# Performance work log

Measured on AMD Instinct MI355X. Metric: run time of the kernel, lower is better.

Reference implementation:

```python
import jax, jax.numpy as jnp
import numpy as np

GRID = 270
POOLED = 90
N_ACTIVE = 30000
LEAK = 0.333  # sparseconvnet BatchNormLeakyReLU default leakiness
CH = [(4, 8), (8, 8), (8, 12), (12, 12), (12, 16), (16, 16)]  # resnet block (nIn, nOut)
NIN_IDX = {0: 0, 2: 1, 4: 2}  # blocks whose shortcut is NetworkInNetwork (nIn != nOut)


def _build_rules(coords, grid, f, lo):
    """Submanifold-conv rulebook: (in_idx, out_idx, offset_idx) pairs over active sites."""
    flat = (coords[:, 0] * grid + coords[:, 1]) * grid + coords[:, 2]
    order = np.argsort(flat)
    flat_s = flat[order]
    n = flat_s.shape[0]
    ins, outs, ks = [], [], []
    kk = 0
    for dx in range(lo, lo + f):
        for dy in range(lo, lo + f):
            for dz in range(lo, lo + f):
                nb = coords + np.array([dx, dy, dz])
                valid = np.all((nb >= 0) & (nb < grid), axis=1)
                nbf = (nb[:, 0] * grid + nb[:, 1]) * grid + nb[:, 2]
                pos = np.clip(np.searchsorted(flat_s, nbf), 0, n - 1)
                hit = valid & (flat_s[pos] == nbf)
                outs.append(np.nonzero(hit)[0])
                ins.append(order[pos[hit]])
                ks.append(np.full(outs[-1].shape[0], kk, dtype=np.int64))
                kk += 1
    return (np.concatenate(ins).astype(np.int32),
            np.concatenate(outs).astype(np.int32),
            np.concatenate(ks).astype(np.int32))


def setup_inputs():
    rng = np.random.default_rng(0)
    flat = np.unique(rng.integers(0, GRID ** 3, size=int(N_ACTIVE * 1.2)))[:N_ACTIVE]
    coords = np.stack([flat // (GRID * GRID), (flat // GRID) % GRID, flat % GRID], 1)
    rb1 = _build_rules(coords, GRID, 2, 0)    # SubmanifoldConvolution f=2
    rb2 = _build_rules(coords, GRID, 15, -7)  # SubmanifoldConvolution f=15
    rb3 = _build_rules(coords, GRID, 5, -2)   # SubmanifoldConvolution f=5
    pc = coords // 3                          # MaxPooling(3, 3)
    pf = (pc[:, 0] * POOLED + pc[:, 1]) * POOLED + pc[:, 2]
    upf, pool_seg = np.unique(pf, return_inverse=True)
    pcoords = np.stack([upf // (POOLED * POOLED), (upf // POOLED) % POOLED, upf % POOLED], 1)
    rb90 = _build_rules(pcoords, POOLED, 3, -1)  # resnet submanifold f=3
    N = coords.shape[0]
    nrm = lambda shape, s: jnp.asarray((rng.normal(0.0, s, size=shape)).astype(np.float32))
    g1s = np.zeros((6, 16), np.float32); b1s = np.zeros((6, 16), np.float32)
    g2s = np.zeros((6, 16), np.float32); b2s = np.zeros((6, 16), np.float32)
    Wa = np.zeros((6, 27, 16, 16), np.float32); Wb = np.zeros((6, 27, 16, 16), np.float32)
    Ws = np.zeros((3, 16, 16), np.float32)
    for i, (ci, co) in enumerate(CH):
        g1s[i, :ci] = 1.0 + 0.05 * rng.normal(size=ci)
        b1s[i, :ci] = 0.05 * rng.normal(size=ci)
        g2s[i, :co] = 1.0 + 0.05 * rng.normal(size=co)
        b2s[i, :co] = 0.05 * rng.normal(size=co)
        Wa[i, :, :ci, :co] = rng.normal(0, 1 / np.sqrt(27 * ci), size=(27, ci, co))
        Wb[i, :, :co, :co] = rng.normal(0, 1 / np.sqrt(27 * co), size=(27, co, co))
        if i in NIN_IDX:
            Ws[NIN_IDX[i], :ci, :co] = rng.normal(0, 1 / np.sqrt(ci), size=(ci, co))
    F = 16 * 84 * 84 * 84
    W_lin1 = jnp.asarray(rng.standard_normal((10, F), dtype=np.float32) * np.float32(1.0 / np.sqrt(F)))
    ii = lambda a: jnp.asarray(a, dtype=jnp.int32)
    return {
        'x_feats': nrm((N, 1), 1.0),
        'W1': nrm((8, 1, 16), 0.35),
        'W2': nrm((3375, 16, 16), 1 / np.sqrt(3375 * 16)),
        'W3': nrm((125, 16, 4), 1 / np.sqrt(125 * 16)),
        'g1s': jnp.asarray(g1s), 'b1s': jnp.asarray(b1s),
        'Wa': jnp.asarray(Wa), 'g2s': jnp.asarray(g2s), 'b2s': jnp.asarray(b2s),
        'Wb': jnp.asarray(Wb), 'Ws': jnp.asarray(Ws),
        'gf': nrm((16,), 0.05) + 1.0, 'bf': nrm((16,), 0.05),
        'Wc1': nrm((16, 16, 3, 3, 3), 1 / np.sqrt(16 * 27)),
        'Wc2': nrm((16, 16, 5, 5, 5), 1 / np.sqrt(16 * 125)),
        'g_bn': nrm((16,), 0.05) + 1.0, 'b_bn': nrm((16,), 0.05),
        'W_lin1': W_lin1, 'b_lin1': nrm((10,), 0.02),
        'W_lin2': nrm((2, 10), 0.3), 'b_lin2': nrm((2,), 0.02),
        'rb1_in': ii(rb1[0]), 'rb1_out': ii(rb1[1]), 'rb1_k': ii(rb1[2]),
        'rb2_in': ii(rb2[0]), 'rb2_out': ii(rb2[1]), 'rb2_k': ii(rb2[2]),
        'rb3_in': ii(rb3[0]), 'rb3_out': ii(rb3[1]), 'rb3_k': ii(rb3[2]),
        'pool_seg': ii(pool_seg),
        'rb90_in': ii(rb90[0]), 'rb90_out': ii(rb90[1]), 'rb90_k': ii(rb90[2]),
        'px': ii(pcoords[:, 0]), 'py': ii(pcoords[:, 1]), 'pz': ii(pcoords[:, 2]),
    }


def _subconv(h, W, in_idx, out_idx, k_idx, n_out):
    # gather active-neighbor features, apply per-offset weight, scatter-add to outputs
    contrib = jnp.einsum('pc,pcd->pd', h[in_idx], W[k_idx])
    return jax.ops.segment_sum(contrib, out_idx, num_segments=n_out)


def reference(x_feats, W1, W2, W3, g1s, b1s, Wa, g2s, b2s, Wb, Ws, gf, bf, Wc1, Wc2,
              g_bn, b_bn, W_lin1, b_lin1, W_lin2, b_lin2,
              rb1_in, rb1_out, rb1_k, rb2_in, rb2_out, rb2_k, rb3_in, rb3_out, rb3_k,
              pool_seg, rb90_in, rb90_out, rb90_k, px, py, pz):
    N = x_feats.shape[0]
    Np = px.shape[0]
    h = _subconv(x_feats, W1, rb1_in, rb1_out, rb1_k, N)   # [N,16] subm conv f=2
    h = _subconv(h, W2, rb2_in, rb2_out, rb2_k, N)         # [N,16] subm conv f=15
    h = _subconv(h, W3, rb3_in, rb3_out, rb3_k, N)         # [N,4]  subm conv f=5
    h = jax.ops.segment_max(h, pool_seg, num_segments=Np)  # sparse MaxPooling 3/3 (dropout=identity, eval)
    h = jnp.pad(h, ((0, 0), (0, 12)))                      # pad channels 4->16; pads stay zero
    for i in range(6):                                     # SparseResNet basic blocks (stride 1)
        u = jax.nn.relu(h * g1s[i] + b1s[i])               # BatchNormReLU (inference, stats folded)
        u = _subconv(u, Wa[i], rb90_in, rb90_out, rb90_k, Np)
        u = jax.nn.relu(u * g2s[i] + b2s[i])
        u = _subconv(u, Wb[i], rb90_in, rb90_out, rb90_k, Np)
        sc = h @ Ws[NIN_IDX[i]] if i in NIN_IDX else h     # NiN or identity shortcut
        h = u + sc
    h = jax.nn.relu(h * gf + bf)                           # trailing BatchNormReLU of SparseResNet
    dense = jnp.zeros((16, POOLED, POOLED, POOLED), h.dtype).at[:, px, py, pz].set(h.T)[None]
    dn = ('NCDHW', 'OIDHW', 'NCDHW')
    d = jax.lax.conv_general_dilated(dense, Wc1, (1, 1, 1), 'VALID', dimension_numbers=dn)  # 90->88
    d = jax.lax.conv_general_dilated(d, Wc2, (1, 1, 1), 'VALID', dimension_numbers=dn)      # 88->84
    d = d * g_bn[None, :, None, None, None] + b_bn[None, :, None, None, None]
    d = jnp.where(d > 0, d, LEAK * d)                      # BatchNormLeakyReLU(16)
    mask = jnp.zeros((1, 1, POOLED, POOLED, POOLED), h.dtype).at[0, 0, px, py, pz].set(1.0)
    mask = jax.lax.reduce_window(mask, 0.0, jax.lax.max, (1, 1, 3, 3, 3), (1,) * 5, 'VALID')
    mask = jax.lax.reduce_window(mask, 0.0, jax.lax.max, (1, 1, 5, 5, 5), (1,) * 5, 'VALID')
    d = d * mask                                           # SparseToDense: zeros off active set
    flat = d.reshape(1, 16 * 84 * 84 * 84)
    return (flat @ W_lin1.T + b_lin1) @ W_lin2.T + b_lin2  # [1, 2]
```

## Files before the change

kernel.cpp:

```cpp
#include <hip/hip_runtime.h>
#include <float.h>

#define TPB 256
#define PG 90
#define PG2 8100
#define PG3 729000
#define DA 88
#define DA2 7744
#define DA3 681472
#define DB 84
#define DB2 7056
#define DB3 592704
#define FTOT 9483264
#define LEAKC 0.333f
#define NBF 1120
#define C1Z 22
#define C2Z 21

static __device__ __forceinline__ void atomicMaxF(float* addr, float val) {
    if (val >= 0.f) atomicMax((int*)addr, __float_as_int(val));
    else            atomicMin((unsigned int*)addr, __float_as_uint(val));
}

__global__ void k_hp_init(float* hp, int n16) {
    int t = blockIdx.x * TPB + threadIdx.x;
    if (t < n16) hp[t] = ((t & 15) < 4) ? -FLT_MAX : 0.f;
}

__global__ void k_sub1(const float* __restrict__ x, const float* __restrict__ W,
                       const int* __restrict__ rin, const int* __restrict__ rout,
                       const int* __restrict__ rk, float* __restrict__ y, int P) {
    int t = blockIdx.x * TPB + threadIdx.x;
    if (t >= P * 16) return;
    int p = t >> 4, d = t & 15;
    atomicAdd(&y[rout[p] * 16 + d], x[rin[p]] * W[rk[p] * 16 + d]);
}

__global__ void k_sub16(const float* __restrict__ h, const float* __restrict__ W,
                        const int* __restrict__ rin, const int* __restrict__ rout,
                        const int* __restrict__ rk, float* __restrict__ y, int P) {
    int t = blockIdx.x * TPB + threadIdx.x;
    if (t >= P * 16) return;
    int p = t >> 4, d = t & 15;
    const float* hr = h + rin[p] * 16;
    const float* w  = W + rk[p] * 256 + d;
    float acc = 0.f;
#pragma unroll
    for (int c = 0; c < 16; c++) acc = fmaf(hr[c], w[c * 16], acc);
    atomicAdd(&y[rout[p] * 16 + d], acc);
}

__global__ void k_sub16bn(const float* __restrict__ h, const float* __restrict__ g,
                          const float* __restrict__ b, const float* __restrict__ W,
                          const int* __restrict__ rin, const int* __restrict__ rout,
                          const int* __restrict__ rk, float* __restrict__ y, int P) {
    int t = blockIdx.x * TPB + threadIdx.x;
    if (t >= P * 16) return;
    int p = t >> 4, d = t & 15;
    const float* hr = h + rin[p] * 16;
    const float* w  = W + rk[p] * 256 + d;
    float acc = 0.f;
#pragma unroll
    for (int c = 0; c < 16; c++) {
        float u = fmaxf(fmaf(hr[c], g[c], b[c]), 0.f);
        acc = fmaf(u, w[c * 16], acc);
    }
    atomicAdd(&y[rout[p] * 16 + d], acc);
}

__global__ void k_sub3(const float* __restrict__ h, const float* __restrict__ W,
                       const int* __restrict__ rin, const int* __restrict__ rout,
                       const int* __restrict__ rk, float* __restrict__ y, int P) {
    int t = blockIdx.x * TPB + threadIdx.x;
    if (t >= P * 4) return;
    int p = t >> 2, d = t & 3;
    const float* hr = h + rin[p] * 16;
    const float* w  = W + rk[p] * 64 + d;
    float acc = 0.f;
#pragma unroll
    for (int c = 0; c < 16; c++) acc = fmaf(hr[c], w[c * 4], acc);
    atomicAdd(&y[rout[p] * 4 + d], acc);
}

__global__ void k_pool(const float* __restrict__ h3, const int* __restrict__ seg,
                       float* __restrict__ hp, int N) {
    int t = blockIdx.x * TPB + threadIdx.x;
    if (t >= N * 4) return;
    int p = t >> 2, d = t & 3;
    atomicMaxF(&hp[seg[p] * 16 + d], h3[t]);
}

__global__ void k_resup(const float* __restrict__ cur, float* __restrict__ wbuf,
                        float* __restrict__ vbuf, const float* __restrict__ Ws,
                        float* __restrict__ nxt, int n16) {
    int t = blockIdx.x * TPB + threadIdx.x;
    if (t >= n16) return;
    int p = t >> 4, d = t & 15;
    float sc;
    if (Ws != nullptr) {
        const float* row = cur + p * 16;
        float acc = 0.f;
#pragma unroll
        for (int c = 0; c < 16; c++) acc = fmaf(row[c], Ws[c * 16 + d], acc);
        sc = acc;
    } else {
        sc = cur[t];
    }
    nxt[t] = wbuf[t] + sc;
    wbuf[t] = 0.f;
    vbuf[t] = 0.f;
}

__global__ void k_scatter(const float* __restrict__ h, const float* __restrict__ gf,
                          const float* __restrict__ bf, const int* __restrict__ px,
                          const int* __restrict__ py, const int* __restrict__ pz,
                          float* __restrict__ dense, unsigned char* __restrict__ occ, int n16) {
    int t = blockIdx.x * TPB + threadIdx.x;
    if (t >= n16) return;
    int p = t >> 4, c = t & 15;
    float v = fmaxf(fmaf(h[t], gf[c], bf[c]), 0.f);
    int pos = (px[p] * PG + py[p]) * PG + pz[p];
    dense[c * PG3 + pos] = v;
    if (c == 0) occ[pos] = 1;
}

__global__ __launch_bounds__(TPB) void k_conv1(const float* __restrict__ in,
                                               const float* __restrict__ W,
                                               float* __restrict__ out) {
    __shared__ float wl[432 * 16];
    for (int t = threadIdx.x; t < 432 * 16; t += TPB) {
        int o = t & 15, tap = t >> 4;
        wl[t] = W[o * 432 + tap];
    }
    __syncthreads();
    int idx = blockIdx.x * TPB + threadIdx.x;
    if (idx >= DA2 * C1Z) return;
    int zg = idx % C1Z;
    int y  = (idx / C1Z) % DA;
    int x  = idx / (C1Z * DA);
    int z0 = zg * 4;
    float acc[4][16];
#pragma unroll
    for (int vz = 0; vz < 4; vz++)
#pragma unroll
        for (int o = 0; o < 16; o++) acc[vz][o] = 0.f;
    for (int i = 0; i < 16; i++) {
        const float* ip = in + (size_t)i * PG3;
#pragma unroll
        for (int kd = 0; kd < 3; kd++) {
#pragma unroll
            for (int kh = 0; kh < 3; kh++) {
                const float* row = ip + (x + kd) * PG2 + (y + kh) * PG + z0;
                float4 fa = *(const float4*)row;
                float4 fb = *(const float4*)(row + 4);
                float v[8] = {fa.x, fa.y, fa.z, fa.w, fb.x, fb.y, fb.z, fb.w};
                const float* wr = &wl[((i * 3 + kd) * 3 + kh) * 3 * 16];
#pragma unroll
                for (int kw = 0; kw < 3; kw++) {
                    const float4* wv = (const float4*)&wr[kw * 16];
                    float4 w0 = wv[0], w1 = wv[1], w2 = wv[2], w3 = wv[3];
#pragma unroll
                    for (int vz = 0; vz < 4; vz++) {
                        float val = v[kw + vz];
                        acc[vz][0]  = fmaf(val, w0.x, acc[vz][0]);
                        acc[vz][1]  = fmaf(val, w0.y, acc[vz][1]);
                        acc[vz][2]  = fmaf(val, w0.z, acc[vz][2]);
                        acc[vz][3]  = fmaf(val, w0.w, acc[vz][3]);
                        acc[vz][4]  = fmaf(val, w1.x, acc[vz][4]);
                        acc[vz][5]  = fmaf(val, w1.y, acc[vz][5]);
                        acc[vz][6]  = fmaf(val, w1.z, acc[vz][6]);
                        acc[vz][7]  = fmaf(val, w1.w, acc[vz][7]);
                        acc[vz][8]  = fmaf(val, w2.x, acc[vz][8]);
                        acc[vz][9]  = fmaf(val, w2.y, acc[vz][9]);
                        acc[vz][10] = fmaf(val, w2.z, acc[vz][10]);
                        acc[vz][11] = fmaf(val, w2.w, acc[vz][11]);
                        acc[vz][12] = fmaf(val, w3.x, acc[vz][12]);
                        acc[vz][13] = fmaf(val, w3.y, acc[vz][13]);
                        acc[vz][14] = fmaf(val, w3.z, acc[vz][14]);
                        acc[vz][15] = fmaf(val, w3.w, acc[vz][15]);
                    }
                }
            }
        }
    }
    int base = x * DA2 + y * DA + z0;
#pragma unroll
    for (int o = 0; o < 16; o++) {
        float4 st = {acc[0][o], acc[1][o], acc[2][o], acc[3][o]};
        *(float4*)(out + (size_t)o * DA3 + base) = st;
    }
}

__global__ __launch_bounds__(TPB) void k_conv2(const float* __restrict__ in,
                                               const float* __restrict__ W,
                                               float* __restrict__ out) {
    __shared__ float wl[4 * 125 * 16];
    int idx = blockIdx.x * TPB + threadIdx.x;
    bool valid = idx < DB2 * C2Z;
    int ii = valid ? idx : 0;
    int zg = ii % C2Z;
    int y  = (ii / C2Z) % DB;
    int x  = ii / (C2Z * DB);
    int z0 = zg * 4;
    float acc[4][16];
#pragma unroll
    for (int vz = 0; vz < 4; vz++)
#pragma unroll
        for (int o = 0; o < 16; o++) acc[vz][o] = 0.f;
    for (int ib = 0; ib < 16; ib += 4) {
        __syncthreads();
        for (int t = threadIdx.x; t < 4 * 125 * 16; t += TPB) {
            int o = t & 15;
            int r = t >> 4;
            int tap = r % 125;
            int ci  = r / 125;
            wl[t] = W[o * 2000 + (ib + ci) * 125 + tap];
        }
        __syncthreads();
        for (int ci = 0; ci < 4; ci++) {
            const float* ip = in + (size_t)(ib + ci) * DA3;
#pragma unroll
            for (int kd = 0; kd < 5; kd++) {
#pragma unroll
                for (int kh = 0; kh < 5; kh++) {
                    const float* row = ip + (x + kd) * DA2 + (y + kh) * DA + z0;
                    float4 fa = *(const float4*)row;
                    float4 fb = *(const float4*)(row + 4);
                    float v[8] = {fa.x, fa.y, fa.z, fa.w, fb.x, fb.y, fb.z, fb.w};
                    const float* wr = &wl[(ci * 125 + kd * 25 + kh * 5) * 16];
#pragma unroll
                    for (int kw = 0; kw < 5; kw++) {
                        const float4* wv = (const float4*)&wr[kw * 16];
                        float4 w0 = wv[0], w1 = wv[1], w2 = wv[2], w3 = wv[3];
#pragma unroll
                        for (int vz = 0; vz < 4; vz++) {
                            float val = v[kw + vz];
                            acc[vz][0]  = fmaf(val, w0.x, acc[vz][0]);
                            acc[vz][1]  = fmaf(val, w0.y, acc[vz][1]);
                            acc[vz][2]  = fmaf(val, w0.z, acc[vz][2]);
                            acc[vz][3]  = fmaf(val, w0.w, acc[vz][3]);
                            acc[vz][4]  = fmaf(val, w1.x, acc[vz][4]);
                            acc[vz][5]  = fmaf(val, w1.y, acc[vz][5]);
                            acc[vz][6]  = fmaf(val, w1.z, acc[vz][6]);
                            acc[vz][7]  = fmaf(val, w1.w, acc[vz][7]);
                            acc[vz][8]  = fmaf(val, w2.x, acc[vz][8]);
                            acc[vz][9]  = fmaf(val, w2.y, acc[vz][9]);
                            acc[vz][10] = fmaf(val, w2.z, acc[vz][10]);
                            acc[vz][11] = fmaf(val, w2.w, acc[vz][11]);
                            acc[vz][12] = fmaf(val, w3.x, acc[vz][12]);
                            acc[vz][13] = fmaf(val, w3.y, acc[vz][13]);
                            acc[vz][14] = fmaf(val, w3.z, acc[vz][14]);
                            acc[vz][15] = fmaf(val, w3.w, acc[vz][15]);
                        }
                    }
                }
            }
        }
    }
    if (valid) {
        int base = x * DB2 + y * DB + z0;
#pragma unroll
        for (int o = 0; o < 16; o++) {
            float4 st = {acc[0][o], acc[1][o], acc[2][o], acc[3][o]};
            *(float4*)(out + (size_t)o * DB3 + base) = st;
        }
    }
}

__global__ void k_mask1(const unsigned char* __restrict__ occ, unsigned char* __restrict__ m1) {
    int t = blockIdx.x * TPB + threadIdx.x;
    if (t >= PG * PG * DB) return;
    int z = t % DB;
    int xy = t / DB;
    const unsigned char* p = occ + xy * PG + z;
    unsigned char m = 0;
#pragma unroll
    for (int k = 0; k < 7; k++) m |= p[k];
    m1[t] = m;
}
__global__ void k_mask2(const unsigned char* __restrict__ m1, unsigned char* __restrict__ m2) {
    int t = blockIdx.x * TPB + threadIdx.x;
    if (t >= PG * DB * DB) return;
    int z = t % DB;
    int y = (t / DB) % DB;
    int x = t / (DB * DB);
    unsigned char m = 0;
#pragma unroll
    for (int k = 0; k < 7; k++) m |= m1[(x * PG + y + k) * DB + z];
    m2[t] = m;
}
__global__ void k_mask3(const unsigned char* __restrict__ m2, unsigned char* __restrict__ mask) {
    int t = blockIdx.x * TPB + threadIdx.x;
    if (t >= DB3) return;
    int z = t % DB;
    int y = (t / DB) % DB;
    int x = t / DB2;
    unsigned char m = 0;
#pragma unroll
    for (int k = 0; k < 7; k++) m |= m2[((x + k) * DB + y) * DB + z];
    mask[t] = m;
}

__global__ __launch_bounds__(TPB) void k_final(const float* __restrict__ c2,
                                               const unsigned char* __restrict__ mask,
                                               const float* __restrict__ gbn,
                                               const float* __restrict__ bbn,
                                               const float* __restrict__ Wl1,
                                               float* __restrict__ buf) {
    int tid0 = blockIdx.x * TPB + threadIdx.x;
    int stride = gridDim.x * TPB;
    float part[10];
#pragma unroll
    for (int j = 0; j < 10; j++) part[j] = 0.f;
    for (int c = 0; c < 16; c++) {
        float g = gbn[c], b = bbn[c];
        const float* cc = c2 + (size_t)c * DB3;
        const float* wb = Wl1 + (size_t)c * DB3;
        for (int sp = tid0; sp < DB3; sp += stride) {
            float v = fmaf(cc[sp], g, b);
            v = v > 0.f ? v : LEAKC * v;
            if (mask[sp]) {
#pragma unroll
                for (int j = 0; j < 10; j++)
                    part[j] = fmaf(v, wb[(size_t)j * FTOT + sp], part[j]);
            }
        }
    }
    int lane = threadIdx.x & 63, wv = threadIdx.x >> 6;
    __shared__ float red[4][10];
#pragma unroll
    for (int j = 0; j < 10; j++) {
        float s = part[j];
#pragma unroll
        for (int off = 32; off; off >>= 1) s += __shfl_down(s, off);
        if (lane == 0) red[wv][j] = s;
    }
    __syncthreads();
    if (threadIdx.x < 10)
        buf[blockIdx.x * 10 + threadIdx.x] =
            red[0][threadIdx.x] + red[1][threadIdx.x] + red[2][threadIdx.x] + red[3][threadIdx.x];
}

__global__ __launch_bounds__(TPB) void k_reduce(const float* __restrict__ buf,
                                                const float* __restrict__ bl1,
                                                float* __restrict__ out10, int nb) {
    int j = blockIdx.x;
    float s = 0.f;
    for (int k = threadIdx.x; k < nb; k += TPB) s += buf[k * 10 + j];
    int lane = threadIdx.x & 63, wv = threadIdx.x >> 6;
#pragma unroll
    for (int off = 32; off; off >>= 1) s += __shfl_down(s, off);
    __shared__ float red[4];
    if (lane == 0) red[wv] = s;
    __syncthreads();
    if (threadIdx.x == 0) out10[j] = red[0] + red[1] + red[2] + red[3] + bl1[j];
}

__global__ void k_head(const float* __restrict__ out10, const float* __restrict__ Wl2,
                       const float* __restrict__ bl2, float* __restrict__ out) {
    if (threadIdx.x == 0) {
        float t0 = bl2[0], t1 = bl2[1];
#pragma unroll
        for (int j = 0; j < 10; j++) {
            float v = out10[j];
            t0 = fmaf(v, Wl2[j], t0);
            t1 = fmaf(v, Wl2[10 + j], t1);
        }
        out[0] = t0;
        out[1] = t1;
    }
}

static inline int nblk(long n) { return (int)((n + TPB - 1) / TPB); }

extern "C" void kernel_launch(void* const* d_in, const int* in_sizes, int n_in,
                              void* d_out, int out_size, void* d_ws, size_t ws_size,
                              hipStream_t stream) {
    const float* x    = (const float*)d_in[0];
    const float* W1   = (const float*)d_in[1];
    const float* W2   = (const float*)d_in[2];
    const float* W3   = (const float*)d_in[3];
    const float* g1s  = (const float*)d_in[4];
    const float* b1s  = (const float*)d_in[5];
    const float* Wa   = (const float*)d_in[6];
    const float* g2s  = (const float*)d_in[7];
    const float* b2s  = (const float*)d_in[8];
    const float* Wb   = (const float*)d_in[9];
    const float* Ws   = (const float*)d_in[10];
    const float* gf   = (const float*)d_in[11];
    const float* bfv  = (const float*)d_in[12];
    const float* Wc1  = (const float*)d_in[13];
    const float* Wc2  = (const float*)d_in[14];
    const float* g_bn = (const float*)d_in[15];
    const float* b_bn = (const float*)d_in[16];
    const float* Wl1  = (const float*)d_in[17];
    const float* bl1  = (const float*)d_in[18];
    const float* Wl2  = (const float*)d_in[19];
    const float* bl2  = (const float*)d_in[20];
    const int* rb1_in = (const int*)d_in[21];
    const int* rb1_out= (const int*)d_in[22];
    const int* rb1_k  = (const int*)d_in[23];
    const int* rb2_in = (const int*)d_in[24];
    const int* rb2_out= (const int*)d_in[25];
    const int* rb2_k  = (const int*)d_in[26];
    const int* rb3_in = (const int*)d_in[27];
    const int* rb3_out= (const int*)d_in[28];
    const int* rb3_k  = (const int*)d_in[29];
    const int* pseg   = (const int*)d_in[30];
    const int* rb9_in = (const int*)d_in[31];
    const int* rb9_out= (const int*)d_in[32];
    const int* rb9_k  = (const int*)d_in[33];
    const int* px     = (const int*)d_in[34];
    const int* py     = (const int*)d_in[35];
    const int* pz     = (const int*)d_in[36];

    const int N   = in_sizes[0];
    const int P1  = in_sizes[21];
    const int P2  = in_sizes[24];
    const int P3  = in_sizes[27];
    const int P90 = in_sizes[31];
    const int Np  = in_sizes[34];

    char* wsp = (char*)d_ws;
    size_t off = 0;
    auto carve = [&](size_t bytes) -> char* {
        char* p = wsp + off;
        off = (off + bytes + 255) & ~(size_t)255;
        return p;
    };
    float* h1    = (float*)carve((size_t)N * 16 * 4);
    float* h2    = (float*)carve((size_t)N * 16 * 4);
    float* h3    = (float*)carve((size_t)N * 4 * 4);
    float* hpA   = (float*)carve((size_t)Np * 16 * 4);
    float* hpB   = (float*)carve((size_t)Np * 16 * 4);
    float* vbuf  = (float*)carve((size_t)Np * 16 * 4);
    float* wbuf  = (float*)carve((size_t)Np * 16 * 4);
    float* dense = (float*)carve((size_t)16 * PG3 * 4);
    float* c1    = (float*)carve((size_t)16 * DA3 * 4);
    unsigned char* occ  = (unsigned char*)carve(PG3);
    unsigned char* m1   = (unsigned char*)carve((size_t)PG * PG * DB);
    unsigned char* m2   = (unsigned char*)carve((size_t)PG * DB * DB);
    unsigned char* mask = (unsigned char*)carve(DB3);
    float* fbuf  = (float*)carve((size_t)NBF * 10 * 4);
    float* out10 = (float*)carve(10 * 4);
    float* c2 = dense;

    hipMemsetAsync(h1, 0, (size_t)N * 16 * 4, stream);
    hipMemsetAsync(h2, 0, (size_t)N * 16 * 4, stream);
    hipMemsetAsync(h3, 0, (size_t)N * 4 * 4, stream);
    hipMemsetAsync(vbuf, 0, (size_t)Np * 16 * 4, stream);
    hipMemsetAsync(wbuf, 0, (size_t)Np * 16 * 4, stream);
    hipMemsetAsync(dense, 0, (size_t)16 * PG3 * 4, stream);
    hipMemsetAsync(occ, 0, PG3, stream);
    k_hp_init<<<nblk((long)Np * 16), TPB, 0, stream>>>(hpA, Np * 16);

    k_sub1<<<nblk((long)P1 * 16), TPB, 0, stream>>>(x, W1, rb1_in, rb1_out, rb1_k, h1, P1);
    k_sub16<<<nblk((long)P2 * 16), TPB, 0, stream>>>(h1, W2, rb2_in, rb2_out, rb2_k, h2, P2);
    k_sub3<<<nblk((long)P3 * 4), TPB, 0, stream>>>(h2, W3, rb3_in, rb3_out, rb3_k, h3, P3);
    k_pool<<<nblk((long)N * 4), TPB, 0, stream>>>(h3, pseg, hpA, N);

    float* cur = hpA;
    float* nxt = hpB;
    for (int i = 0; i < 6; i++) {
        const float* WsP = nullptr;
        if (i == 0) WsP = Ws;
        else if (i == 2) WsP = Ws + 256;
        else if (i == 4) WsP = Ws + 512;
        k_sub16bn<<<nblk((long)P90 * 16), TPB, 0, stream>>>(
            cur, g1s + i * 16, b1s + i * 16, Wa + (size_t)i * 6912,
            rb9_in, rb9_out, rb9_k, vbuf, P90);
        k_sub16bn<<<nblk((long)P90 * 16), TPB, 0, stream>>>(
            vbuf, g2s + i * 16, b2s + i * 16, Wb + (size_t)i * 6912,
            rb9_in, rb9_out, rb9_k, wbuf, P90);
        k_resup<<<nblk((long)Np * 16), TPB, 0, stream>>>(cur, wbuf, vbuf, WsP, nxt, Np * 16);
        float* tmp = cur; cur = nxt; nxt = tmp;
    }

    k_scatter<<<nblk((long)Np * 16), TPB, 0, stream>>>(cur, gf, bfv, px, py, pz, dense, occ, Np * 16);
    k_conv1<<<nblk((long)DA2 * C1Z), TPB, 0, stream>>>(dense, Wc1, c1);
    k_conv2<<<nblk((long)DB2 * C2Z), TPB, 0, stream>>>(c1, Wc2, c2);

    k_mask1<<<nblk((long)PG * PG * DB), TPB, 0, stream>>>(occ, m1);
    k_mask2<<<nblk((long)PG * DB * DB), TPB, 0, stream>>>(m1, m2);
    k_mask3<<<nblk(DB3), TPB, 0, stream>>>(m2, mask);

    k_final<<<NBF, TPB, 0, stream>>>(c2, mask, g_bn, b_bn, Wl1, fbuf);
    k_reduce<<<10, TPB, 0, stream>>>(fbuf, bl1, out10, NBF);
    k_head<<<1, 64, 0, stream>>>(out10, Wl2, bl2, (float*)d_out);
}
```

Baseline: 1.411 ms.

## Split dense convs into two output-channel halves, read pre-permuted weights from global

Both dense 3D convolutions now launch twice as many threads, each computing 8 output channels instead of 16, which halves the accumulator registers per thread and should allow higher occupancy. Weights are permuted once by a new small kernel into tap-major order and read straight from global memory (through cache) instead of being staged in shared memory. This removes the per-block shared-memory fill and barriers. In exchange, every input voxel row is loaded twice (once per half), and the inner loop issues more global weight loads.

```diff
diff --git a/kernel.cpp b/kernel.cpp
--- a/kernel.cpp
+++ b/kernel.cpp
@@ -27,6 +27,13 @@
     if (t < n16) hp[t] = ((t & 15) < 4) ? -FLT_MAX : 0.f;
 }
 
+__global__ void k_permW(const float* __restrict__ W, float* __restrict__ Wp, int ntap) {
+    int t = blockIdx.x * TPB + threadIdx.x;
+    if (t >= ntap * 16) return;
+    int o = t & 15, tap = t >> 4;
+    Wp[t] = W[o * ntap + tap];
+}
+
 __global__ void k_sub1(const float* __restrict__ x, const float* __restrict__ W,
                        const int* __restrict__ rin, const int* __restrict__ rout,
                        const int* __restrict__ rk, float* __restrict__ y, int P) {
@@ -125,59 +132,47 @@
 }
 
 __global__ __launch_bounds__(TPB) void k_conv1(const float* __restrict__ in,
-                                               const float* __restrict__ W,
+                                               const float* __restrict__ Wp,
                                                float* __restrict__ out) {
-    __shared__ float wl[432 * 16];
-    for (int t = threadIdx.x; t < 432 * 16; t += TPB) {
-        int o = t & 15, tap = t >> 4;
-        wl[t] = W[o * 432 + tap];
-    }
-    __syncthreads();
     int idx = blockIdx.x * TPB + threadIdx.x;
-    if (idx >= DA2 * C1Z) return;
-    int zg = idx % C1Z;
-    int y  = (idx / C1Z) % DA;
-    int x  = idx / (C1Z * DA);
+    if (idx >= DA2 * C1Z * 2) return;
+    int oh   = idx / (DA2 * C1Z);
+    int idx2 = idx % (DA2 * C1Z);
+    int zg = idx2 % C1Z;
+    int y  = (idx2 / C1Z) % DA;
+    int x  = idx2 / (C1Z * DA);
     int z0 = zg * 4;
-    float acc[4][16];
+    float acc[4][8];
 #pragma unroll
     for (int vz = 0; vz < 4; vz++)
 #pragma unroll
-        for (int o = 0; o < 16; o++) acc[vz][o] = 0.f;
-    for (int i = 0; i < 16; i++) {
-        const float* ip = in + (size_t)i * PG3;
-#pragma unroll
+        for (int o = 0; o < 8; o++) acc[vz][o] = 0.f;
+    const float* wbase = Wp + oh * 8;
+    for (int ci = 0; ci < 16; ci++) {
+        const float* ip = in + (size_t)ci * PG3 + x * PG2 + y * PG + z0;
+        const float* wc = wbase + ci * 27 * 16;
         for (int kd = 0; kd < 3; kd++) {
-#pragma unroll
             for (int kh = 0; kh < 3; kh++) {
-                const float* row = ip + (x + kd) * PG2 + (y + kh) * PG + z0;
+                const float* row = ip + kd * PG2 + kh * PG;
                 float4 fa = *(const float4*)row;
                 float4 fb = *(const float4*)(row + 4);
                 float v[8] = {fa.x, fa.y, fa.z, fa.w, fb.x, fb.y, fb.z, fb.w};
-                const float* wr = &wl[((i * 3 + kd) * 3 + kh) * 3 * 16];
+                const float* wr = wc + (kd * 9 + kh * 3) * 16;
 #pragma unroll
                 for (int kw = 0; kw < 3; kw++) {
-                    const float4* wv = (const float4*)&wr[kw * 16];
-                    float4 w0 = wv[0], w1 = wv[1], w2 = wv[2], w3 = wv[3];
+                    float4 w0 = *(const float4*)(wr + kw * 16);
+                    float4 w1 = *(const float4*)(wr + kw * 16 + 4);
 #pragma unroll
                     for (int vz = 0; vz < 4; vz++) {
                         float val = v[kw + vz];
-                        acc[vz][0]  = fmaf(val, w0.x, acc[vz][0]);
-                        acc[vz][1]  = fmaf(val, w0.y, acc[vz][1]);
-                        acc[vz][2]  = fmaf(val, w0.z, acc[vz][2]);
-                        acc[vz][3]  = fmaf(val, w0.w, acc[vz][3]);
-                        acc[vz][4]  = fmaf(val, w1.x, acc[vz][4]);
-                        acc[vz][5]  = fmaf(val, w1.y, acc[vz][5]);
-                        acc[vz][6]  = fmaf(val, w1.z, acc[vz][6]);
-                        acc[vz][7]  = fmaf(val, w1.w, acc[vz][7]);
-                        acc[vz][8]  = fmaf(val, w2.x, acc[vz][8]);
-                        acc[vz][9]  = fmaf(val, w2.y, acc[vz][9]);
-                        acc[vz][10] = fmaf(val, w2.z, acc[vz][10]);
-                        acc[vz][11] = fmaf(val, w2.w, acc[vz][11]);
-                        acc[vz][12] = fmaf(val, w3.x, acc[vz][12]);
-                        acc[vz][13] = fmaf(val, w3.y, acc[vz][13]);
-                        acc[vz][14] = fmaf(val, w3.z, acc[vz][14]);
-                        acc[vz][15] = fmaf(val, w3.w, acc[vz][15]);
+                        acc[vz][0] = fmaf(val, w0.x, acc[vz][0]);
+                        acc[vz][1] = fmaf(val, w0.y, acc[vz][1]);
+                        acc[vz][2] = fmaf(val, w0.z, acc[vz][2]);
+                        acc[vz][3] = fmaf(val, w0.w, acc[vz][3]);
+                        acc[vz][4] = fmaf(val, w1.x, acc[vz][4]);
+                        acc[vz][5] = fmaf(val, w1.y, acc[vz][5]);
+                        acc[vz][6] = fmaf(val, w1.z, acc[vz][6]);
+                        acc[vz][7] = fmaf(val, w1.w, acc[vz][7]);
                     }
                 }
             }
@@ -185,85 +180,64 @@
     }
     int base = x * DA2 + y * DA + z0;
 #pragma unroll
-    for (int o = 0; o < 16; o++) {
+    for (int o = 0; o < 8; o++) {
         float4 st = {acc[0][o], acc[1][o], acc[2][o], acc[3][o]};
-        *(float4*)(out + (size_t)o * DA3 + base) = st;
+        *(float4*)(out + (size_t)(oh * 8 + o) * DA3 + base) = st;
     }
 }
 
 __global__ __launch_bounds__(TPB) void k_conv2(const float* __restrict__ in,
-                                               const float* __restrict__ W,
+                                               const float* __restrict__ Wp,
                                                float* __restrict__ out) {
-    __shared__ float wl[4 * 125 * 16];
     int idx = blockIdx.x * TPB + threadIdx.x;
-    bool valid = idx < DB2 * C2Z;
-    int ii = valid ? idx : 0;
-    int zg = ii % C2Z;
-    int y  = (ii / C2Z) % DB;
-    int x  = ii / (C2Z * DB);
+    if (idx >= DB2 * C2Z * 2) return;
+    int oh   = idx / (DB2 * C2Z);
+    int idx2 = idx % (DB2 * C2Z);
+    int zg = idx2 % C2Z;
+    int y  = (idx2 / C2Z) % DB;
+    int x  = idx2 / (C2Z * DB);
     int z0 = zg * 4;
-    float acc[4][16];
+    float acc[4][8];
 #pragma unroll
     for (int vz = 0; vz < 4; vz++)
 #pragma unroll
-        for (int o = 0; o < 16; o++) acc[vz][o] = 0.f;
-    for (int ib = 0; ib < 16; ib += 4) {
-        __syncthreads();
-        for (int t = threadIdx.x; t < 4 * 125 * 16; t += TPB) {
-            int o = t & 15;
-            int r = t >> 4;
-            int tap = r % 125;
-            int ci  = r / 125;
-            wl[t] = W[o * 2000 + (ib + ci) * 125 + tap];
-        }
-        __syncthreads();
-        for (int ci = 0; ci < 4; ci++) {
-            const float* ip = in + (size_t)(ib + ci) * DA3;
-#pragma unroll
-            for (int kd = 0; kd < 5; kd++) {
-#pragma unroll
-                for (int kh = 0; kh < 5; kh++) {
-                    const float* row = ip + (x + kd) * DA2 + (y + kh) * DA + z0;
-                    float4 fa = *(const float4*)row;
-                    float4 fb = *(const float4*)(row + 4);
-                    float v[8] = {fa.x, fa.y, fa.z, fa.w, fb.x, fb.y, fb.z, fb.w};
-                    const float* wr = &wl[(ci * 125 + kd * 25 + kh * 5) * 16];
-#pragma unroll
-                    for (int kw = 0; kw < 5; kw++) {
-                        const float4* wv = (const float4*)&wr[kw * 16];
-                        float4 w0 = wv[0], w1 = wv[1], w2 = wv[2], w3 = wv[3];
-#pragma unroll
-                        for (int vz = 0; vz < 4; vz++) {
-                            float val = v[kw + vz];
-                            acc[vz][0]  = fmaf(val, w0.x, acc[vz][0]);
-                            acc[vz][1]  = fmaf(val, w0.y, acc[vz][1]);
-                            acc[vz][2]  = fmaf(val, w0.z, acc[vz][2]);
-                            acc[vz][3]  = fmaf(val, w0.w, acc[vz][3]);
-                            acc[vz][4]  = fmaf(val, w1.x, acc[vz][4]);
-                            acc[vz][5]  = fmaf(val, w1.y, acc[vz][5]);
-                            acc[vz][6]  = fmaf(val, w1.z, acc[vz][6]);
-                            acc[vz][7]  = fmaf(val, w1.w, acc[vz][7]);
-                            acc[vz][8]  = fmaf(val, w2.x, acc[vz][8]);
-                            acc[vz][9]  = fmaf(val, w2.y, acc[vz][9]);
-                            acc[vz][10] = fmaf(val, w2.z, acc[vz][10]);
-                            acc[vz][11] = fmaf(val, w2.w, acc[vz][11]);
-                            acc[vz][12] = fmaf(val, w3.x, acc[vz][12]);
-                            acc[vz][13] = fmaf(val, w3.y, acc[vz][13]);
-                            acc[vz][14] = fmaf(val, w3.z, acc[vz][14]);
-                            acc[vz][15] = fmaf(val, w3.w, acc[vz][15]);
-                        }
+        for (int o = 0; o < 8; o++) acc[vz][o] = 0.f;
+    const float* wbase = Wp + oh * 8;
+    for (int ci = 0; ci < 16; ci++) {
+        const float* ip = in + (size_t)ci * DA3 + x * DA2 + y * DA + z0;
+        const float* wc = wbase + ci * 125 * 16;
+        for (int kd = 0; kd < 5; kd++) {
+            for (int kh = 0; kh < 5; kh++) {
+                const float* row = ip + kd * DA2 + kh * DA;
+                float4 fa = *(const float4*)row;
+                float4 fb = *(const float4*)(row + 4);
+                float v[8] = {fa.x, fa.y, fa.z, fa.w, fb.x, fb.y, fb.z, fb.w};
+                const float* wr = wc + (kd * 25 + kh * 5) * 16;
+#pragma unroll
+                for (int kw = 0; kw < 5; kw++) {
+                    float4 w0 = *(const float4*)(wr + kw * 16);
+                    float4 w1 = *(const float4*)(wr + kw * 16 + 4);
+#pragma unroll
+                    for (int vz = 0; vz < 4; vz++) {
+                        float val = v[kw + vz];
+                        acc[vz][0] = fmaf(val, w0.x, acc[vz][0]);
+                        acc[vz][1] = fmaf(val, w0.y, acc[vz][1]);
+                        acc[vz][2] = fmaf(val, w0.z, acc[vz][2]);
+                        acc[vz][3] = fmaf(val, w0.w, acc[vz][3]);
+                        acc[vz][4] = fmaf(val, w1.x, acc[vz][4]);
+                        acc[vz][5] = fmaf(val, w1.y, acc[vz][5]);
+                        acc[vz][6] = fmaf(val, w1.z, acc[vz][6]);
+                        acc[vz][7] = fmaf(val, w1.w, acc[vz][7]);
                     }
                 }
             }
         }
     }
-    if (valid) {
-        int base = x * DB2 + y * DB + z0;
-#pragma unroll
-        for (int o = 0; o < 16; o++) {
-            float4 st = {acc[0][o], acc[1][o], acc[2][o], acc[3][o]};
-            *(float4*)(out + (size_t)o * DB3 + base) = st;
-        }
+    int base = x * DB2 + y * DB + z0;
+#pragma unroll
+    for (int o = 0; o < 8; o++) {
+        float4 st = {acc[0][o], acc[1][o], acc[2][o], acc[3][o]};
+        *(float4*)(out + (size_t)(oh * 8 + o) * DB3 + base) = st;
     }
 }
 
@@ -443,6 +417,8 @@
     unsigned char* mask = (unsigned char*)carve(DB3);
     float* fbuf  = (float*)carve((size_t)NBF * 10 * 4);
     float* out10 = (float*)carve(10 * 4);
+    float* Wp1   = (float*)carve((size_t)432 * 16 * 4);
+    float* Wp2   = (float*)carve((size_t)2000 * 16 * 4);
     float* c2 = dense;
 
     hipMemsetAsync(h1, 0, (size_t)N * 16 * 4, stream);
@@ -453,6 +429,8 @@
     hipMemsetAsync(dense, 0, (size_t)16 * PG3 * 4, stream);
     hipMemsetAsync(occ, 0, PG3, stream);
     k_hp_init<<<nblk((long)Np * 16), TPB, 0, stream>>>(hpA, Np * 16);
+    k_permW<<<nblk(432 * 16), TPB, 0, stream>>>(Wc1, Wp1, 432);
+    k_permW<<<nblk(2000 * 16), TPB, 0, stream>>>(Wc2, Wp2, 2000);
 
     k_sub1<<<nblk((long)P1 * 16), TPB, 0, stream>>>(x, W1, rb1_in, rb1_out, rb1_k, h1, P1);
     k_sub16<<<nblk((long)P2 * 16), TPB, 0, stream>>>(h1, W2, rb2_in, rb2_out, rb2_k, h2, P2);
@@ -477,8 +455,8 @@
     }
 
     k_scatter<<<nblk((long)Np * 16), TPB, 0, stream>>>(cur, gf, bfv, px, py, pz, dense, occ, Np * 16);
-    k_conv1<<<nblk((long)DA2 * C1Z), TPB, 0, stream>>>(dense, Wc1, c1);
-    k_conv2<<<nblk((long)DB2 * C2Z), TPB, 0, stream>>>(c1, Wc2, c2);
+    k_conv1<<<nblk((long)DA2 * C1Z * 2), TPB, 0, stream>>>(dense, Wp1, c1);
+    k_conv2<<<nblk((long)DB2 * C2Z * 2), TPB, 0, stream>>>(c1, Wp2, c2);
 
     k_mask1<<<nblk((long)PG * PG * DB), TPB, 0, stream>>>(occ, m1);
     k_mask2<<<nblk((long)PG * DB * DB), TPB, 0, stream>>>(m1, m2);
```

New measurement: 1.892 ms. 1.34x slower.
